# Performance work log

Hardware: AMD Instinct MI355X
Metric: run time of the kernel (lower is better)

Reference implementation:

```python
import jax, jax.numpy as jnp
import numpy as np

N = 512          # max_nodes
H = 256          # hidden_dim
L = 4            # num_layers
T = 100          # num_timesteps
NE = N * (N - 1) // 2  # 130816 upper-triangular edges

# --- cosine noise schedule (computed in float64 numpy, stored as float32) ---
_s = 0.008
_steps = np.arange(T + 1, dtype=np.float64)
_ab = np.cos((_steps / T + _s) / (1 + _s) * np.pi / 2) ** 2
_ab = _ab / _ab[0]
_betas = np.clip(1.0 - _ab[1:] / _ab[:-1], None, 0.999).astype(np.float32)
_alphas = 1.0 - _betas
_alpha_bar = np.cumprod(_alphas).astype(np.float32)
SQRT_AB = jnp.asarray(np.sqrt(_alpha_bar), dtype=jnp.float32)
SQRT_OMAB = jnp.asarray(np.sqrt(1.0 - _alpha_bar), dtype=jnp.float32)
IU, JU = np.triu_indices(N, k=1)  # upper-triangular edge indices


def silu(x):
    return x * jax.nn.sigmoid(x)


def layernorm(x, g, b, eps=1e-5):
    mu = jnp.mean(x, axis=-1, keepdims=True)
    var = jnp.mean(jnp.square(x - mu), axis=-1, keepdims=True)
    return (x - mu) / jnp.sqrt(var + eps) * g + b


def setup_inputs() -> dict:
    key = jax.random.key(0)
    ks = jax.random.split(key, 16)
    B = 32
    p = lambda k, shape: jax.random.normal(k, shape, dtype=jnp.float32) * 0.02
    return {
        "adj_0": jax.random.normal(ks[0], (B, N, N), dtype=jnp.float32),
        "noise": jax.random.normal(ks[1], (B, N, N), dtype=jnp.float32),
        # time embedding MLP: Linear(1,H), SiLU, Linear(H,H)
        "te_W1": p(ks[2], (1, H)), "te_b1": jnp.zeros((H,), jnp.float32),
        "te_W2": p(ks[3], (H, H)), "te_b2": jnp.zeros((H,), jnp.float32),
        # input projection Linear(N, H)
        "ip_W": p(ks[4], (N, H)), "ip_b": jnp.zeros((H,), jnp.float32),
        # per-layer params stacked on leading L axis
        "msg_W": p(ks[5], (L, H, H)), "msg_b": jnp.zeros((L, H), jnp.float32),
        "upd_W": p(ks[6], (L, 2 * H, H)), "upd_b": jnp.zeros((L, H), jnp.float32),
        "ln_g": jnp.ones((L, H), jnp.float32), "ln_b": jnp.zeros((L, H), jnp.float32),
        "tp_W": p(ks[7], (L, H, H)), "tp_b": jnp.zeros((L, H), jnp.float32),
        # output projection: Linear(H,H), SiLU, Linear(H, NE)
        "op_W1": p(ks[8], (H, H)), "op_b1": jnp.zeros((H,), jnp.float32),
        "op_W2": p(ks[9], (H, NE)), "op_b2": jnp.zeros((NE,), jnp.float32),
        "t": jax.random.randint(ks[10], (32,), 0, T),
    }


def reference(adj_0, noise, te_W1, te_b1, te_W2, te_b2, ip_W, ip_b,
              msg_W, msg_b, upd_W, upd_b, ln_g, ln_b, tp_W, tp_b,
              op_W1, op_b1, op_W2, op_b2, t):
    # q_sample: noisy adjacency at timestep t
    adj_t = SQRT_AB[t][:, None, None] * adj_0 + SQRT_OMAB[t][:, None, None] * noise
    # time embedding
    tf = (t.astype(jnp.float32) / T)[:, None]               # [B,1]
    t_emb = silu(tf @ te_W1 + te_b1) @ te_W2 + te_b2        # [B,H]
    # input projection
    h = adj_t @ ip_W + ip_b                                  # [B,N,H]
    # adjacency normalization is identical across layers -> hoist
    adj_norm = adj_t / (jnp.sum(jnp.abs(adj_t), axis=-1, keepdims=True) + 1.0)
    for l in range(L):
        msg = jnp.einsum('bij,bjh->bih', adj_norm, h @ msg_W[l] + msg_b[l])
        t_bias = (t_emb @ tp_W[l] + tp_b[l])[:, None, :]     # [B,1,H]
        h_new = jnp.concatenate([h, msg], axis=-1) @ upd_W[l] + upd_b[l] + t_bias
        h = layernorm(h_new + h, ln_g[l], ln_b[l])
    h_graph = jnp.sum(h, axis=1)                             # [B,H]
    noise_pred = silu(h_graph @ op_W1 + op_b1) @ op_W2 + op_b2  # [B,NE]
    # MSE against the upper-triangular entries of the true noise
    target = noise[:, IU, JU]                                # [B,NE]
    loss = jnp.mean(jnp.square(noise_pred - target))
    return loss
```

## Files before the change

kernel.cpp:

```cpp
#include <hip/hip_runtime.h>
#include <math.h>

#define NN 512
#define HH 256
#define BB 32
#define NE 130816

typedef unsigned short ushort_t;
typedef unsigned int u32;
using short8  = __attribute__((ext_vector_type(8))) short;
using floatx4 = __attribute__((ext_vector_type(4))) float;

typedef __attribute__((address_space(3))) u32* lds_u32p;
typedef const __attribute__((address_space(1))) u32* glb_u32p;

__device__ inline unsigned short f2bf(float f) {
    unsigned int u = __float_as_uint(f);
    unsigned int r = (u + 0x7fffu + ((u >> 16) & 1u)) >> 16;
    return (unsigned short)r;
}
__device__ inline float bf2f(unsigned short x) {
    return __uint_as_float(((unsigned int)x) << 16);
}

__device__ inline float wave_reduce_sum(float v) {
#pragma unroll
    for (int o = 32; o > 0; o >>= 1) v += __shfl_xor(v, o, 64);
    return v;
}
__device__ inline float block_reduce_sum256(float v, float* red) {
    v = wave_reduce_sum(v);
    int w = threadIdx.x >> 6;
    if ((threadIdx.x & 63) == 0) red[w] = v;
    __syncthreads();
    v = red[0] + red[1] + red[2] + red[3];
    __syncthreads();
    return v;
}

__global__ void init_kernel(float* __restrict__ sched, float* __restrict__ out) {
    __shared__ float alpha_s[100];
    int tid = threadIdx.x;
    if (tid < 100) {
        const double PI_H = 3.14159265358979323846 * 0.5;
        double f1 = (((double)tid / 100.0) + 0.008) / 1.008 * PI_H;
        double f2 = (((double)(tid + 1) / 100.0) + 0.008) / 1.008 * PI_H;
        double c1 = cos(f1), c2 = cos(f2);
        double beta = 1.0 - (c2 * c2) / (c1 * c1);
        if (beta > 0.999) beta = 0.999;
        alpha_s[tid] = 1.0f - (float)beta;
    }
    __syncthreads();
    if (tid == 0) {
        out[0] = 0.0f;
        float cum = 1.0f;
        for (int k = 0; k < 100; k++) {
            cum *= alpha_s[k];
            sched[k]       = sqrtf(cum);
            sched[100 + k] = sqrtf(1.0f - cum);
        }
    }
}

__global__ __launch_bounds__(256) void temb1_kernel(
    const float* __restrict__ te_W1, const float* __restrict__ te_b1,
    const float* __restrict__ te_W2, const float* __restrict__ te_b2,
    const int* __restrict__ t, float* __restrict__ emb_out) {
    const int b = blockIdx.x, cb = blockIdx.y * 64, tid = threadIdx.x;
    __shared__ float hid[HH];
    __shared__ float part[4][64];
    float tf = (float)t[b] / 100.0f;
    float z = tf * te_W1[tid] + te_b1[tid];
    hid[tid] = z / (1.0f + expf(-z));
    __syncthreads();
    const int col = tid & 63, kc = tid >> 6;
    float a = 0.0f;
#pragma unroll 8
    for (int k0 = 0; k0 < 64; k0++) {
        int k = kc * 64 + k0;
        a = fmaf(hid[k], te_W2[k * HH + cb + col], a);
    }
    part[kc][col] = a;
    __syncthreads();
    if (kc == 0) {
        float o = part[0][col] + part[1][col] + part[2][col] + part[3][col] + te_b2[cb + col];
        emb_out[b * HH + cb + col] = o;
    }
}

__global__ __launch_bounds__(256) void temb2_kernel(
    const float* __restrict__ emb, const float* __restrict__ tp_W,
    const float* __restrict__ tp_b, float* __restrict__ tbias_out) {
    const int b = blockIdx.x;
    const int l = blockIdx.y >> 2, cb = (blockIdx.y & 3) * 64;
    const int tid = threadIdx.x;
    __shared__ float es[HH];
    __shared__ float part[4][64];
    es[tid] = emb[b * HH + tid];
    __syncthreads();
    const int col = tid & 63, kc = tid >> 6;
    const float* W = tp_W + l * HH * HH;
    float a = 0.0f;
#pragma unroll 8
    for (int k0 = 0; k0 < 64; k0++) {
        int k = kc * 64 + k0;
        a = fmaf(es[k], W[k * HH + cb + col], a);
    }
    part[kc][col] = a;
    __syncthreads();
    if (kc == 0) {
        float o = part[0][col] + part[1][col] + part[2][col] + part[3][col]
                + tp_b[l * HH + cb + col];
        tbias_out[l * (BB * HH) + b * HH + cb + col] = o;
    }
}

__global__ __launch_bounds__(256) void adj_kernel(
    const float* __restrict__ adj0, const float* __restrict__ noise,
    const int* __restrict__ t, const float* __restrict__ sched,
    ushort_t* __restrict__ adjt_bf, float* __restrict__ invrs) {
    __shared__ float red[4];
    const int bid = blockIdx.x;
    const int b = bid >> 9;
    const int ts = t[b];
    const float sab = sched[ts], som = sched[100 + ts];
    const size_t base = (size_t)bid * NN;
    const int tid = threadIdx.x;
    const int j = tid * 2;
    float2 a0 = *(const float2*)&adj0[base + j];
    float2 n0 = *(const float2*)&noise[base + j];
    float x = fmaf(sab, a0.x, som * n0.x);
    float y = fmaf(sab, a0.y, som * n0.y);
    *(u32*)&adjt_bf[base + j] = (u32)f2bf(x) | ((u32)f2bf(y) << 16);
    float s = fabsf(x) + fabsf(y);
    s = block_reduce_sum256(s, red);
    if (tid == 0) invrs[bid] = 1.0f / (s + 1.0f);
}

__global__ __launch_bounds__(256) void wcvt_kernel(
    const float* __restrict__ ip_W, const float* __restrict__ msg_W,
    const float* __restrict__ upd_W,
    ushort_t* __restrict__ ipWT, ushort_t* __restrict__ msgWbf,
    ushort_t* __restrict__ updWT) {
    const int z = blockIdx.z;
    const int r0 = blockIdx.y * 32, c0 = blockIdx.x * 32;
    const int tr = threadIdx.x >> 5, tc = threadIdx.x & 31;
    if (z >= 1 && z <= 4) {
        const float* src = msg_W + (z - 1) * 65536;
        ushort_t* dst = msgWbf + (z - 1) * 65536;
        if (r0 >= 256) return;
#pragma unroll
        for (int s = 0; s < 32; s += 8)
            dst[(size_t)(r0 + tr + s) * 256 + c0 + tc] =
                f2bf(src[(size_t)(r0 + tr + s) * 256 + c0 + tc]);
        return;
    }
    const float* src; ushort_t* dst; int R;
    if (z == 0) { src = ip_W;                     dst = ipWT;                     R = 512; }
    else        { src = upd_W + (z - 5) * 131072; dst = updWT + (z - 5) * 131072; R = 512; }
    __shared__ float T[32][33];
#pragma unroll
    for (int s = 0; s < 32; s += 8)
        T[tr + s][tc] = src[(size_t)(r0 + tr + s) * 256 + c0 + tc];
    __syncthreads();
#pragma unroll
    for (int s = 0; s < 32; s += 8)
        dst[(size_t)(c0 + tr + s) * R + r0 + tc] = f2bf(T[tc][tr + s]);
}

__global__ __launch_bounds__(256) void bfv_kernel(
    const float* __restrict__ msg_b, const float* __restrict__ upd_W,
    float* __restrict__ bfv) {
    const int l = blockIdx.x, n = threadIdx.x;
    float a = 0.0f;
#pragma unroll 8
    for (int j = 0; j < 256; j++)
        a = fmaf(msg_b[l * 256 + j], upd_W[(size_t)l * 131072 + (size_t)(256 + j) * 256 + n], a);
    bfv[l * 256 + n] = a;
}

__global__ __launch_bounds__(256, 2) void gemm_bf16(
    int K, int nsplit,
    const ushort_t* __restrict__ A, int lda, long long aStrideZ,
    const ushort_t* __restrict__ BT, int ldbt,
    const ushort_t* __restrict__ BT2, int ldbt2,
    long long btStrideZ, long long bstride,
    const float* __restrict__ bias, const float* __restrict__ bias2,
    const float* __restrict__ scale,
    const float* __restrict__ tbias, const ushort_t* __restrict__ resid,
    const ushort_t* __restrict__ part1,
    float* __restrict__ Cf, ushort_t* __restrict__ Cb, ushort_t* __restrict__ CbT,
    long long cStrideZ) {
    __shared__ ushort_t As[128 * 32];
    __shared__ ushort_t Bs[64 * 32];
    __shared__ ushort_t Ts[64 * 136];
    const int row0 = blockIdx.x * 128;
    const int n0 = blockIdx.y * 64;
    const int z = blockIdx.z;
    const int tid = threadIdx.x;
    const int lane = tid & 63;
    const int w = tid >> 6;
    const int l15 = lane & 15, quad = lane >> 4;
    const int wm = (w >> 1) * 64, wn = (w & 1) * 32;

    const bool reg2 = (n0 >= nsplit);
    const ushort_t* BTu = reg2 ? BT2 : BT;
    const int ldbtu = reg2 ? ldbt2 : ldbt;
    const int n0u = reg2 ? (n0 - nsplit) : n0;
    const ushort_t* Az = A + (size_t)z * aStrideZ;
    const ushort_t* Bp = BTu + (size_t)z * btStrideZ + (size_t)(row0 >> 9) * (size_t)bstride;

    const int srow = lane >> 2;
    const int gkoff = (((lane & 3) ^ (lane >> 4)) << 3);
    const int swz = ((quad ^ ((l15 >> 2) & 3)) << 3);

    floatx4 acc[4][2];
#pragma unroll
    for (int i = 0; i < 4; i++)
#pragma unroll
        for (int j = 0; j < 2; j++) {
            acc[i][j][0] = 0.0f; acc[i][j][1] = 0.0f;
            acc[i][j][2] = 0.0f; acc[i][j][3] = 0.0f;
        }

    for (int kc = 0; kc < K; kc += 32) {
#pragma unroll
        for (int r = 0; r < 2; r++) {
            const int lbase = (r * 4 + w) * 16;
            const ushort_t* gpA = Az + (size_t)(row0 + lbase + srow) * lda + kc + gkoff;
            __builtin_amdgcn_global_load_lds((glb_u32p)(const void*)gpA,
                                             (lds_u32p)(void*)&As[lbase * 32], 16, 0, 0);
        }
        {
            const int lbase = w * 16;
            const ushort_t* gpB = Bp + (size_t)(n0u + lbase + srow) * ldbtu + kc + gkoff;
            __builtin_amdgcn_global_load_lds((glb_u32p)(const void*)gpB,
                                             (lds_u32p)(void*)&Bs[lbase * 32], 16, 0, 0);
        }
        __syncthreads();

        short8 af[4], bfr[2];
#pragma unroll
        for (int tm = 0; tm < 4; tm++)
            af[tm] = *(const short8*)&As[(wm + tm * 16 + l15) * 32 + swz];
#pragma unroll
        for (int tn = 0; tn < 2; tn++)
            bfr[tn] = *(const short8*)&Bs[(wn + tn * 16 + l15) * 32 + swz];
#pragma unroll
        for (int tm = 0; tm < 4; tm++)
#pragma unroll
            for (int tn = 0; tn < 2; tn++)
                acc[tm][tn] = __builtin_amdgcn_mfma_f32_16x16x32_bf16(
                    af[tm], bfr[tn], acc[tm][tn], 0, 0, 0);
        __syncthreads();
    }

    if (reg2) {
#pragma unroll
        for (int tm = 0; tm < 4; tm++)
#pragma unroll
            for (int tn = 0; tn < 2; tn++)
#pragma unroll
                for (int r = 0; r < 4; r++) {
                    const int ml = wm + tm * 16 + quad * 4 + r;
                    const int cl = wn + tn * 16 + l15;
                    float v = acc[tm][tn][r];
                    if (bias2) v += bias2[n0u + cl];
                    Ts[cl * 136 + ml] = f2bf(v);
                }
        __syncthreads();
        const int cl = tid >> 2, ch = (tid & 3) * 32;
        const int b = row0 >> 9;
        ushort_t* dst = CbT + (size_t)b * NN * HH + (size_t)(n0u + cl) * NN + (row0 & 511) + ch;
        uint4 u0 = *(const uint4*)&Ts[cl * 136 + ch];
        uint4 u1 = *(const uint4*)&Ts[cl * 136 + ch + 8];
        uint4 u2 = *(const uint4*)&Ts[cl * 136 + ch + 16];
        uint4 u3 = *(const uint4*)&Ts[cl * 136 + ch + 24];
        *(uint4*)(dst)      = u0;
        *(uint4*)(dst + 8)  = u1;
        *(uint4*)(dst + 16) = u2;
        *(uint4*)(dst + 24) = u3;
        return;
    }

#pragma unroll
    for (int tm = 0; tm < 4; tm++)
#pragma unroll
        for (int tn = 0; tn < 2; tn++) {
#pragma unroll
            for (int r = 0; r < 4; r++) {
                const int row = row0 + wm + tm * 16 + quad * 4 + r;
                const int col = n0 + wn + tn * 16 + l15;
                float v = acc[tm][tn][r];
                if (scale) v *= scale[row];
                if (bias) v += bias[col];
                if (part1) v += bf2f(part1[(size_t)row * HH + col]);
                if (tbias) v += tbias[((row >> 9) << 8) + col] + bf2f(resid[(size_t)row * HH + col]);
                if (Cf) Cf[(size_t)row * HH + col] = v;
                if (Cb) Cb[(size_t)z * cStrideZ + (size_t)row * HH + col] = f2bf(v);
            }
        }
}

__global__ __launch_bounds__(256) void ln_kernel(
    const float* __restrict__ pre, const float* __restrict__ g,
    const float* __restrict__ b, ushort_t* __restrict__ h_bf) {
    __shared__ float red[4];
    const size_t base = (size_t)blockIdx.x * HH;
    const int tid = threadIdx.x;
    float x = pre[base + tid];
    float mu = block_reduce_sum256(x, red) * (1.0f / HH);
    float d = x - mu;
    float var = block_reduce_sum256(d * d, red) * (1.0f / HH);
    h_bf[base + tid] = f2bf(d * rsqrtf(var + 1e-5f) * g[tid] + b[tid]);
}

__global__ __launch_bounds__(256) void psum_kernel(
    const ushort_t* __restrict__ h_bf, float* __restrict__ partial) {
    const int b = blockIdx.x, ch = blockIdx.y, tid = threadIdx.x;
    const ushort_t* hp = h_bf + ((size_t)b * NN + ch * 32) * HH;
    float s = 0.0f;
#pragma unroll
    for (int i = 0; i < 32; i++) s += bf2f(hp[i * HH + tid]);
    partial[(((size_t)b * 16 + ch) << 8) + tid] = s;
}

__global__ __launch_bounds__(256) void final_kernel(
    const float* __restrict__ partial, const float* __restrict__ op_W1,
    const float* __restrict__ op_b1, float* __restrict__ sT) {
    int b = blockIdx.x, tid = threadIdx.x;
    __shared__ float hg[HH];
    float acc = 0.0f;
#pragma unroll
    for (int c = 0; c < 16; c++) acc += partial[(((size_t)b * 16 + c) << 8) + tid];
    hg[tid] = acc;
    __syncthreads();
    float o = op_b1[tid];
#pragma unroll 8
    for (int k = 0; k < HH; k++) o = fmaf(hg[k], op_W1[k * HH + tid], o);
    sT[tid * BB + b] = o / (1.0f + expf(-o));
}

__global__ __launch_bounds__(256) void loss_kernel(
    const float* __restrict__ sT, const float* __restrict__ op_W2,
    const float* __restrict__ op_b2, const float* __restrict__ noise,
    float* __restrict__ out) {
    __shared__ float red[4];
    const int tid = threadIdx.x;
    const int e = blockIdx.x * 256 + tid;
    float lsum = 0.0f;
    float acc[32];
#pragma unroll
    for (int b = 0; b < 32; b++) acc[b] = 0.0f;
    const float* w2 = op_W2 + e;
#pragma unroll 8
    for (int h = 0; h < 256; h++) {
        float wv = w2[(size_t)h * NE];
        const float* sr = sT + h * BB;
#pragma unroll
        for (int b = 0; b < 32; b++) acc[b] = fmaf(sr[b], wv, acc[b]);
    }
    int i = (int)((1023.0 - sqrt(1046529.0 - 8.0 * (double)e)) * 0.5);
    if (i < 0) i = 0;
    if (i > 510) i = 510;
    while (i > 0 && (i * (1023 - i)) / 2 > e) --i;
    while (((i + 1) * (1022 - i)) / 2 <= e) ++i;
    int j = i + 1 + (e - (i * (1023 - i)) / 2);
    const float pb = op_b2[e];
    const float* np = noise + (size_t)i * NN + j;
#pragma unroll
    for (int b = 0; b < 32; b++) {
        float d = acc[b] + pb - np[(size_t)b * NN * NN];
        lsum += d * d;
    }
    lsum *= (1.0f / (32.0f * (float)NE));
    lsum = block_reduce_sum256(lsum, red);
    if (tid == 0) atomicAdd(out, lsum);
}

extern "C" void kernel_launch(void* const* d_in, const int* in_sizes, int n_in,
                              void* d_out, int out_size, void* d_ws, size_t ws_size,
                              hipStream_t stream) {
    const float* adj0  = (const float*)d_in[0];
    const float* noise = (const float*)d_in[1];
    const float* te_W1 = (const float*)d_in[2];
    const float* te_b1 = (const float*)d_in[3];
    const float* te_W2 = (const float*)d_in[4];
    const float* te_b2 = (const float*)d_in[5];
    const float* ip_W  = (const float*)d_in[6];
    const float* ip_b  = (const float*)d_in[7];
    const float* msg_W = (const float*)d_in[8];
    const float* msg_b = (const float*)d_in[9];
    const float* upd_W = (const float*)d_in[10];
    const float* upd_b = (const float*)d_in[11];
    const float* ln_g  = (const float*)d_in[12];
    const float* ln_b  = (const float*)d_in[13];
    const float* tp_W  = (const float*)d_in[14];
    const float* tp_b  = (const float*)d_in[15];
    const float* op_W1 = (const float*)d_in[16];
    const float* op_b1 = (const float*)d_in[17];
    const float* op_W2 = (const float*)d_in[18];
    const float* op_b2 = (const float*)d_in[19];
    const int*   t     = (const int*)d_in[20];
    float* out = (float*)d_out;

    float* ws = (float*)d_ws;
    float* sched   = ws;
    float* tbias   = ws + 256;
    float* invrs   = ws + 33024;
    float* sbuf    = ws + 49408;
    float* embb    = ws + 57600;
    float* bfv     = ws + 65792;
    float* partial = ws + 66816;
    float* pre     = ws + 197888;
    ushort_t* bfb  = (ushort_t*)(ws + 4392192);
    ushort_t* adjt_bf = bfb;
    ushort_t* h_bf    = bfb + 8388608;
    ushort_t* part1   = bfb + 12582912;
    ushort_t* hm2T    = bfb + 16777216;
    ushort_t* ipWT    = bfb + 20971520;
    ushort_t* msgWbf  = bfb + 21102592;
    ushort_t* updWT   = bfb + 21364736;
    ushort_t* WfT     = bfb + 21889024;

    const int NS_OFF = 1 << 30;

    init_kernel<<<1, 128, 0, stream>>>(sched, out);
    wcvt_kernel<<<dim3(8, 16, 9), 256, 0, stream>>>(ip_W, msg_W, upd_W, ipWT, msgWbf, updWT);
    bfv_kernel<<<4, 256, 0, stream>>>(msg_b, upd_W, bfv);
    temb1_kernel<<<dim3(32, 4), 256, 0, stream>>>(te_W1, te_b1, te_W2, te_b2, t, embb);
    temb2_kernel<<<dim3(32, 16), 256, 0, stream>>>(embb, tp_W, tp_b, tbias);
    adj_kernel<<<BB * NN, 256, 0, stream>>>(adj0, noise, t, sched, adjt_bf, invrs);

    gemm_bf16<<<dim3(2, 4, 4), 256, 0, stream>>>(
        256, NS_OFF,
        updWT + 256, 512, 131072,
        msgWbf, 256, nullptr, 0, 65536, 0,
        nullptr, nullptr, nullptr, nullptr, nullptr, nullptr,
        nullptr, WfT, nullptr, 65536);

    gemm_bf16<<<dim3(128, 4), 256, 0, stream>>>(
        512, NS_OFF,
        adjt_bf, 512, 0,
        ipWT, 512, nullptr, 0, 0, 0,
        ip_b, nullptr, nullptr, nullptr, nullptr, nullptr,
        nullptr, h_bf, nullptr, 0);

    for (int l = 0; l < 4; l++) {
        gemm_bf16<<<dim3(128, 8), 256, 0, stream>>>(
            256, 256,
            h_bf, 256, 0,
            updWT + l * 131072, 512,
            WfT + l * 65536, 256, 0, 0,
            nullptr, bfv + l * 256, nullptr, nullptr, nullptr, nullptr,
            nullptr, part1, hm2T, 0);
        gemm_bf16<<<dim3(128, 4), 256, 0, stream>>>(
            512, NS_OFF,
            adjt_bf, 512, 0,
            hm2T, 512, nullptr, 0, 0, (long long)(HH * NN),
            upd_b + l * HH, nullptr, invrs,
            tbias + l * BB * HH, h_bf, part1,
            pre, nullptr, nullptr, 0);
        ln_kernel<<<BB * NN, 256, 0, stream>>>(pre, ln_g + l * HH, ln_b + l * HH, h_bf);
    }
    psum_kernel<<<dim3(32, 16), 256, 0, stream>>>(h_bf, partial);
    final_kernel<<<32, 256, 0, stream>>>(partial, op_W1, op_b1, sbuf);
    loss_kernel<<<511, 256, 0, stream>>>(sbuf, op_W2, op_b2, noise, out);
}
```

Before: 636.3 us.

## Fuse LayerNorm into the aggregation GEMM epilogue and vectorize adj kernel

Adds a new full-row GEMM kernel (32 rows × 256 cols per block) for the adjacency-aggregation step. Its epilogue computes the residual, biases and LayerNorm in-register, which removes the fp32 pre-LN buffer and the separate ln_kernel launch per layer. The adj kernel now handles one row per wave with float4 loads and a wave reduction. The loss kernel prefetches 16 W2 values at once, and the generic GEMM grid is reordered so n varies fastest. The trade-off is fewer blocks per aggregation GEMM (512), and variance is computed as E[x²]−mu², which is less numerically stable.

```diff
diff --git a/kernel.cpp b/kernel.cpp
--- a/kernel.cpp
+++ b/kernel.cpp
@@ -119,22 +119,30 @@
     const float* __restrict__ adj0, const float* __restrict__ noise,
     const int* __restrict__ t, const float* __restrict__ sched,
     ushort_t* __restrict__ adjt_bf, float* __restrict__ invrs) {
-    __shared__ float red[4];
-    const int bid = blockIdx.x;
-    const int b = bid >> 9;
+    const int row = blockIdx.x * 4 + (threadIdx.x >> 6);
+    const int lane = threadIdx.x & 63;
+    const int b = row >> 9;
     const int ts = t[b];
     const float sab = sched[ts], som = sched[100 + ts];
-    const size_t base = (size_t)bid * NN;
-    const int tid = threadIdx.x;
-    const int j = tid * 2;
-    float2 a0 = *(const float2*)&adj0[base + j];
-    float2 n0 = *(const float2*)&noise[base + j];
-    float x = fmaf(sab, a0.x, som * n0.x);
-    float y = fmaf(sab, a0.y, som * n0.y);
-    *(u32*)&adjt_bf[base + j] = (u32)f2bf(x) | ((u32)f2bf(y) << 16);
-    float s = fabsf(x) + fabsf(y);
-    s = block_reduce_sum256(s, red);
-    if (tid == 0) invrs[bid] = 1.0f / (s + 1.0f);
+    const size_t base = (size_t)row * NN + lane * 8;
+    float4 a0 = *(const float4*)(adj0 + base);
+    float4 a1 = *(const float4*)(adj0 + base + 4);
+    float4 q0 = *(const float4*)(noise + base);
+    float4 q1 = *(const float4*)(noise + base + 4);
+    float v0 = fmaf(sab, a0.x, som * q0.x), v1 = fmaf(sab, a0.y, som * q0.y);
+    float v2 = fmaf(sab, a0.z, som * q0.z), v3 = fmaf(sab, a0.w, som * q0.w);
+    float v4 = fmaf(sab, a1.x, som * q1.x), v5 = fmaf(sab, a1.y, som * q1.y);
+    float v6 = fmaf(sab, a1.z, som * q1.z), v7 = fmaf(sab, a1.w, som * q1.w);
+    uint4 pk;
+    pk.x = (u32)f2bf(v0) | ((u32)f2bf(v1) << 16);
+    pk.y = (u32)f2bf(v2) | ((u32)f2bf(v3) << 16);
+    pk.z = (u32)f2bf(v4) | ((u32)f2bf(v5) << 16);
+    pk.w = (u32)f2bf(v6) | ((u32)f2bf(v7) << 16);
+    *(uint4*)(adjt_bf + base) = pk;
+    float s = fabsf(v0) + fabsf(v1) + fabsf(v2) + fabsf(v3)
+            + fabsf(v4) + fabsf(v5) + fabsf(v6) + fabsf(v7);
+    s = wave_reduce_sum(s);
+    if (lane == 0) invrs[row] = 1.0f / (s + 1.0f);
 }
 
 __global__ __launch_bounds__(256) void wcvt_kernel(
@@ -179,23 +187,18 @@
     bfv[l * 256 + n] = a;
 }
 
-__global__ __launch_bounds__(256, 2) void gemm_bf16(
+__global__ __launch_bounds__(256, 2) void gemm_tile(
     int K, int nsplit,
     const ushort_t* __restrict__ A, int lda, long long aStrideZ,
     const ushort_t* __restrict__ BT, int ldbt,
-    const ushort_t* __restrict__ BT2, int ldbt2,
-    long long btStrideZ, long long bstride,
+    const ushort_t* __restrict__ BT2, int ldbt2, long long btStrideZ,
     const float* __restrict__ bias, const float* __restrict__ bias2,
-    const float* __restrict__ scale,
-    const float* __restrict__ tbias, const ushort_t* __restrict__ resid,
-    const ushort_t* __restrict__ part1,
-    float* __restrict__ Cf, ushort_t* __restrict__ Cb, ushort_t* __restrict__ CbT,
-    long long cStrideZ) {
+    ushort_t* __restrict__ Cb, ushort_t* __restrict__ CbT, long long cStrideZ) {
     __shared__ ushort_t As[128 * 32];
     __shared__ ushort_t Bs[64 * 32];
     __shared__ ushort_t Ts[64 * 136];
-    const int row0 = blockIdx.x * 128;
-    const int n0 = blockIdx.y * 64;
+    const int n0 = blockIdx.x * 64;
+    const int row0 = blockIdx.y * 128;
     const int z = blockIdx.z;
     const int tid = threadIdx.x;
     const int lane = tid & 63;
@@ -208,7 +211,7 @@
     const int ldbtu = reg2 ? ldbt2 : ldbt;
     const int n0u = reg2 ? (n0 - nsplit) : n0;
     const ushort_t* Az = A + (size_t)z * aStrideZ;
-    const ushort_t* Bp = BTu + (size_t)z * btStrideZ + (size_t)(row0 >> 9) * (size_t)bstride;
+    const ushort_t* Bp = BTu + (size_t)z * btStrideZ;
 
     const int srow = lane >> 2;
     const int gkoff = (((lane & 3) ^ (lane >> 4)) << 3);
@@ -292,27 +295,138 @@
                 const int row = row0 + wm + tm * 16 + quad * 4 + r;
                 const int col = n0 + wn + tn * 16 + l15;
                 float v = acc[tm][tn][r];
-                if (scale) v *= scale[row];
                 if (bias) v += bias[col];
-                if (part1) v += bf2f(part1[(size_t)row * HH + col]);
-                if (tbias) v += tbias[((row >> 9) << 8) + col] + bf2f(resid[(size_t)row * HH + col]);
-                if (Cf) Cf[(size_t)row * HH + col] = v;
-                if (Cb) Cb[(size_t)z * cStrideZ + (size_t)row * HH + col] = f2bf(v);
+                Cb[(size_t)z * cStrideZ + (size_t)row * HH + col] = f2bf(v);
             }
         }
 }
 
-__global__ __launch_bounds__(256) void ln_kernel(
-    const float* __restrict__ pre, const float* __restrict__ g,
-    const float* __restrict__ b, ushort_t* __restrict__ h_bf) {
-    __shared__ float red[4];
-    const size_t base = (size_t)blockIdx.x * HH;
+__global__ __launch_bounds__(256, 2) void gemm_preln(
+    const ushort_t* __restrict__ A,
+    const ushort_t* __restrict__ BT,
+    const float* __restrict__ invrs,
+    const float* __restrict__ upd_b,
+    const float* __restrict__ tbias,
+    const ushort_t* __restrict__ part1,
+    const float* __restrict__ ln_g, const float* __restrict__ ln_b,
+    ushort_t* __restrict__ h_bf) {
+    __shared__ ushort_t As[32 * 32];
+    __shared__ ushort_t Bs[256 * 32];
+    __shared__ float rsum[32][4];
+    __shared__ float rsq[32][4];
+    const int row0 = blockIdx.x * 32;
+    const int b = row0 >> 9;
     const int tid = threadIdx.x;
-    float x = pre[base + tid];
-    float mu = block_reduce_sum256(x, red) * (1.0f / HH);
-    float d = x - mu;
-    float var = block_reduce_sum256(d * d, red) * (1.0f / HH);
-    h_bf[base + tid] = f2bf(d * rsqrtf(var + 1e-5f) * g[tid] + b[tid]);
+    const int lane = tid & 63;
+    const int w = tid >> 6;
+    const int l15 = lane & 15, quad = lane >> 4;
+    const int wn = w * 64;
+    const int srow = lane >> 2;
+    const int gkoff = (((lane & 3) ^ (lane >> 4)) << 3);
+    const int swz = ((quad ^ ((l15 >> 2) & 3)) << 3);
+    const ushort_t* Bb = BT + (size_t)b * (HH * NN);
+
+    floatx4 acc[2][4];
+#pragma unroll
+    for (int i = 0; i < 2; i++)
+#pragma unroll
+        for (int j = 0; j < 4; j++) {
+            acc[i][j][0] = 0.0f; acc[i][j][1] = 0.0f;
+            acc[i][j][2] = 0.0f; acc[i][j][3] = 0.0f;
+        }
+
+    for (int kc = 0; kc < 512; kc += 32) {
+        if (w < 2) {
+            const ushort_t* gpA = A + (size_t)(row0 + w * 16 + srow) * 512 + kc + gkoff;
+            __builtin_amdgcn_global_load_lds((glb_u32p)(const void*)gpA,
+                                             (lds_u32p)(void*)&As[(w * 16) * 32], 16, 0, 0);
+        }
+#pragma unroll
+        for (int r = 0; r < 4; r++) {
+            const int nb = r * 64 + w * 16;
+            const ushort_t* gpB = Bb + (size_t)(nb + srow) * 512 + kc + gkoff;
+            __builtin_amdgcn_global_load_lds((glb_u32p)(const void*)gpB,
+                                             (lds_u32p)(void*)&Bs[nb * 32], 16, 0, 0);
+        }
+        __syncthreads();
+
+        short8 af[2], bfr[4];
+#pragma unroll
+        for (int tm = 0; tm < 2; tm++)
+            af[tm] = *(const short8*)&As[(tm * 16 + l15) * 32 + swz];
+#pragma unroll
+        for (int tn = 0; tn < 4; tn++)
+            bfr[tn] = *(const short8*)&Bs[(wn + tn * 16 + l15) * 32 + swz];
+#pragma unroll
+        for (int tm = 0; tm < 2; tm++)
+#pragma unroll
+            for (int tn = 0; tn < 4; tn++)
+                acc[tm][tn] = __builtin_amdgcn_mfma_f32_16x16x32_bf16(
+                    af[tm], bfr[tn], acc[tm][tn], 0, 0, 0);
+        __syncthreads();
+    }
+
+    float ev[2][4][4];
+    float ps[2][4], pq[2][4];
+#pragma unroll
+    for (int tm = 0; tm < 2; tm++)
+#pragma unroll
+        for (int r = 0; r < 4; r++) { ps[tm][r] = 0.0f; pq[tm][r] = 0.0f; }
+#pragma unroll
+    for (int tm = 0; tm < 2; tm++)
+#pragma unroll
+        for (int r = 0; r < 4; r++) {
+            const int row = row0 + tm * 16 + quad * 4 + r;
+            const float iv = invrs[row];
+#pragma unroll
+            for (int tn = 0; tn < 4; tn++) {
+                const int col = wn + tn * 16 + l15;
+                float v = acc[tm][tn][r] * iv + upd_b[col] + tbias[(b << 8) + col]
+                        + bf2f(part1[(size_t)row * HH + col])
+                        + bf2f(h_bf[(size_t)row * HH + col]);
+                ev[tm][tn][r] = v;
+                ps[tm][r] += v;
+                pq[tm][r] += v * v;
+            }
+        }
+#pragma unroll
+    for (int o = 1; o < 16; o <<= 1) {
+#pragma unroll
+        for (int tm = 0; tm < 2; tm++)
+#pragma unroll
+            for (int r = 0; r < 4; r++) {
+                ps[tm][r] += __shfl_xor(ps[tm][r], o, 64);
+                pq[tm][r] += __shfl_xor(pq[tm][r], o, 64);
+            }
+    }
+    if (l15 == 0) {
+#pragma unroll
+        for (int tm = 0; tm < 2; tm++)
+#pragma unroll
+            for (int r = 0; r < 4; r++) {
+                rsum[tm * 16 + quad * 4 + r][w] = ps[tm][r];
+                rsq[tm * 16 + quad * 4 + r][w] = pq[tm][r];
+            }
+    }
+    __syncthreads();
+#pragma unroll
+    for (int tm = 0; tm < 2; tm++)
+#pragma unroll
+        for (int r = 0; r < 4; r++) {
+            const int rl = tm * 16 + quad * 4 + r;
+            const int row = row0 + rl;
+            float s = rsum[rl][0] + rsum[rl][1] + rsum[rl][2] + rsum[rl][3];
+            float q = rsq[rl][0] + rsq[rl][1] + rsq[rl][2] + rsq[rl][3];
+            float mu = s * (1.0f / HH);
+            float var = q * (1.0f / HH) - mu * mu;
+            float rs = rsqrtf(var + 1e-5f);
+#pragma unroll
+            for (int tn = 0; tn < 4; tn++) {
+                const int col = wn + tn * 16 + l15;
+                float o = (ev[tm][tn][r] - mu) * rs * ln_g[col] + ln_b[col];
+                h_bf[(size_t)row * HH + col] = f2bf(o);
+            }
+        }
 }
 
 __global__ __launch_bounds__(256) void psum_kernel(
@@ -353,12 +467,17 @@
 #pragma unroll
     for (int b = 0; b < 32; b++) acc[b] = 0.0f;
     const float* w2 = op_W2 + e;
-#pragma unroll 8
-    for (int h = 0; h < 256; h++) {
-        float wv = w2[(size_t)h * NE];
-        const float* sr = sT + h * BB;
-#pragma unroll
-        for (int b = 0; b < 32; b++) acc[b] = fmaf(sr[b], wv, acc[b]);
+    for (int h0 = 0; h0 < 256; h0 += 16) {
+        float wv[16];
+#pragma unroll
+        for (int u = 0; u < 16; u++)
+            wv[u] = w2[(size_t)(h0 + u) * NE];
+#pragma unroll
+        for (int u = 0; u < 16; u++) {
+            const float* sr = sT + (h0 + u) * BB;
+#pragma unroll
+            for (int b = 0; b < 32; b++) acc[b] = fmaf(sr[b], wv[u], acc[b]);
+        }
     }
     int i = (int)((1023.0 - sqrt(1046529.0 - 8.0 * (double)e)) * 0.5);
     if (i < 0) i = 0;
@@ -412,8 +531,7 @@
     float* embb    = ws + 57600;
     float* bfv     = ws + 65792;
     float* partial = ws + 66816;
-    float* pre     = ws + 197888;
-    ushort_t* bfb  = (ushort_t*)(ws + 4392192);
+    ushort_t* bfb  = (ushort_t*)(ws + 197888);
     ushort_t* adjt_bf = bfb;
     ushort_t* h_bf    = bfb + 8388608;
     ushort_t* part1   = bfb + 12582912;
@@ -430,38 +548,34 @@
     bfv_kernel<<<4, 256, 0, stream>>>(msg_b, upd_W, bfv);
     temb1_kernel<<<dim3(32, 4), 256, 0, stream>>>(te_W1, te_b1, te_W2, te_b2, t, embb);
     temb2_kernel<<<dim3(32, 16), 256, 0, stream>>>(embb, tp_W, tp_b, tbias);
-    adj_kernel<<<BB * NN, 256, 0, stream>>>(adj0, noise, t, sched, adjt_bf, invrs);
-
-    gemm_bf16<<<dim3(2, 4, 4), 256, 0, stream>>>(
+    adj_kernel<<<4096, 256, 0, stream>>>(adj0, noise, t, sched, adjt_bf, invrs);
+
+    gemm_tile<<<dim3(4, 2, 4), 256, 0, stream>>>(
         256, NS_OFF,
         updWT + 256, 512, 131072,
-        msgWbf, 256, nullptr, 0, 65536, 0,
-        nullptr, nullptr, nullptr, nullptr, nullptr, nullptr,
-        nullptr, WfT, nullptr, 65536);
-
-    gemm_bf16<<<dim3(128, 4), 256, 0, stream>>>(
+        msgWbf, 256, nullptr, 0, 65536,
+        nullptr, nullptr,
+        WfT, nullptr, 65536);
+
+    gemm_tile<<<dim3(4, 128), 256, 0, stream>>>(
         512, NS_OFF,
         adjt_bf, 512, 0,
-        ipWT, 512, nullptr, 0, 0, 0,
-        ip_b, nullptr, nullptr, nullptr, nullptr, nullptr,
-        nullptr, h_bf, nullptr, 0);
+        ipWT, 512, nullptr, 0, 0,
+        ip_b, nullptr,
+        h_bf, nullptr, 0);
 
     for (int l = 0; l < 4; l++) {
-        gemm_bf16<<<dim3(128, 8), 256, 0, stream>>>(
+        gemm_tile<<<dim3(8, 128), 256, 0, stream>>>(
             256, 256,
             h_bf, 256, 0,
             updWT + l * 131072, 512,
-            WfT + l * 65536, 256, 0, 0,
-            nullptr, bfv + l * 256, nullptr, nullptr, nullptr, nullptr,
-            nullptr, part1, hm2T, 0);
-        gemm_bf16<<<dim3(128, 4), 256, 0, stream>>>(
-            512, NS_OFF,
-            adjt_bf, 512, 0,
-            hm2T, 512, nullptr, 0, 0, (long long)(HH * NN),
-            upd_b + l * HH, nullptr, invrs,
-            tbias + l * BB * HH, h_bf, part1,
-            pre, nullptr, nullptr, 0);
-        ln_kernel<<<BB * NN, 256, 0, stream>>>(pre, ln_g + l * HH, ln_b + l * HH, h_bf);
+            WfT + l * 65536, 256, 0,
+            nullptr, bfv + l * 256,
+            part1, hm2T, 0);
+        gemm_preln<<<512, 256, 0, stream>>>(
+            adjt_bf, hm2T, invrs,
+            upd_b + l * HH, tbias + l * BB * HH, part1,
+            ln_g + l * HH, ln_b + l * HH, h_bf);
     }
     psum_kernel<<<dim3(32, 16), 256, 0, stream>>>(h_bf, partial);
     final_kernel<<<32, 256, 0, stream>>>(partial, op_W1, op_b1, sbuf);
```

Measured after the change: 542.4 us. 14.8% less time.
